# Performance work log

Measured on AMD Instinct MI355X. Metric: run time of the kernel, lower is better.

## Reference

```python
import jax, jax.numpy as jnp
import numpy as np
import math

EMBED_DIM = 1024
N_HEADS = 16
HEAD_DIM = EMBED_DIM // N_HEADS


def setup_inputs() -> dict:
    key = jax.random.key(0)
    k1, k2, k3, k4 = jax.random.split(key, 4)
    B, S, D = 2, 2048, EMBED_DIM
    inputs = jax.random.normal(k1, (B, S, D), dtype=jnp.float32)
    cross_embeddings = jax.random.normal(k2, (B, S, D), dtype=jnp.float32)
    # learned params
    ln_weight = jnp.ones((D,), dtype=jnp.float32)
    ln_bias = jnp.zeros((D,), dtype=jnp.float32)
    # nn.Linear weights are [out_features, in_features]
    kv_weight = jax.random.normal(k3, (2 * D, D), dtype=jnp.float32) * (1.0 / math.sqrt(D))
    q_weight = jax.random.normal(k4, (D, D), dtype=jnp.float32) * (1.0 / math.sqrt(D))
    return {
        "inputs": inputs,
        "cross_embeddings": cross_embeddings,
        "ln_weight": ln_weight,
        "ln_bias": ln_bias,
        "kv_weight": kv_weight,
        "q_weight": q_weight,
    }


def _layer_norm(x, w, b, eps=1e-5):
    mu = jnp.mean(x, axis=-1, keepdims=True)
    var = jnp.mean(jnp.square(x - mu), axis=-1, keepdims=True)
    return (x - mu) * jax.lax.rsqrt(var + eps) * w + b


def reference(inputs, cross_embeddings, ln_weight, ln_bias, kv_weight, q_weight):
    B, S, D = inputs.shape
    H, Dh = N_HEADS, HEAD_DIM
    resid = inputs
    x = _layer_norm(inputs, ln_weight, ln_bias)
    # kv projection on cross embeddings: y = x @ W^T
    kv = jnp.einsum('bsd,ed->bse', cross_embeddings, kv_weight)  # [B,S,2D]
    k, v = kv[..., :D], kv[..., D:]
    q = jnp.einsum('bsd,ed->bse', x, q_weight)  # [B,S,D]
    q = q.reshape(B, S, H, Dh).transpose(0, 2, 1, 3)  # [B,H,S,Dh]
    k = k.reshape(B, S, H, Dh).transpose(0, 2, 1, 3)
    v = v.reshape(B, S, H, Dh).transpose(0, 2, 1, 3)
    attn = jnp.einsum('bhqd,bhkd->bhqk', q, k) / math.sqrt(Dh)
    attn = jax.nn.softmax(attn, axis=-1)
    out = jnp.einsum('bhqk,bhkd->bhqd', attn, v)  # [B,H,S,Dh]
    out = out.transpose(0, 2, 1, 3).reshape(B, S, D)
    return out + resid
```

## Files before the change

### kernel.cpp

```cpp
#include <hip/hip_runtime.h>
#include <cstdint>
#include <cstddef>


typedef float  f32x4  __attribute__((ext_vector_type(4)));
typedef __bf16 bf16x8 __attribute__((ext_vector_type(8)));
typedef __bf16 bf16x4 __attribute__((ext_vector_type(4)));
typedef __bf16 bf16x2 __attribute__((ext_vector_type(2)));

#define MFMA16(a, b, c) __builtin_amdgcn_mfma_f32_16x16x32_bf16((a), (b), (c), 0, 0, 0)

__device__ __forceinline__ void gll16(const void* g, void* l) {
  __builtin_amdgcn_global_load_lds(
      (const __attribute__((address_space(1))) unsigned int*)g,
      (__attribute__((address_space(3))) unsigned int*)l, 16, 0, 0);
}

__device__ __forceinline__ bf16x2 split2(float x) {
  bf16x2 r;
  __bf16 hh = (__bf16)x;
  r[0] = hh;
  r[1] = (__bf16)(x - (float)hh);
  return r;
}

__global__ __launch_bounds__(256) void prep_kernel(
    const float* __restrict__ x, const float* __restrict__ w, const float* __restrict__ b,
    __bf16* __restrict__ xh, __bf16* __restrict__ xl,
    const float* __restrict__ c,  __bf16* __restrict__ ch, __bf16* __restrict__ cl,
    const float* __restrict__ kw, __bf16* __restrict__ kh, __bf16* __restrict__ kl,
    const float* __restrict__ qw, __bf16* __restrict__ qh, __bf16* __restrict__ ql)
{
  const int tid = threadIdx.x;
  if (blockIdx.x < 4096) {
    const int row = blockIdx.x;
    const float4 v = *reinterpret_cast<const float4*>(x + (size_t)row * 1024 + tid * 4);
    float s  = v.x + v.y + v.z + v.w;
    float s2 = v.x * v.x + v.y * v.y + v.z * v.z + v.w * v.w;
#pragma unroll
    for (int o = 1; o < 64; o <<= 1) { s += __shfl_xor(s, o, 64); s2 += __shfl_xor(s2, o, 64); }
    __shared__ float red[8];
    const int wv = tid >> 6, ln = tid & 63;
    if (ln == 0) { red[wv] = s; red[4 + wv] = s2; }
    __syncthreads();
    s  = red[0] + red[1] + red[2] + red[3];
    s2 = red[4] + red[5] + red[6] + red[7];
    const float mu = s * (1.f / 1024.f);
    const float rs = rsqrtf(s2 * (1.f / 1024.f) - mu * mu + 1e-5f);
    const float4 wv4 = *reinterpret_cast<const float4*>(w + tid * 4);
    const float4 bv4 = *reinterpret_cast<const float4*>(b + tid * 4);
    float o4[4] = {(v.x - mu) * rs * wv4.x + bv4.x, (v.y - mu) * rs * wv4.y + bv4.y,
                   (v.z - mu) * rs * wv4.z + bv4.z, (v.w - mu) * rs * wv4.w + bv4.w};
    bf16x4 h, l;
#pragma unroll
    for (int i = 0; i < 4; ++i) { bf16x2 hl = split2(o4[i]); h[i] = hl[0]; l[i] = hl[1]; }
    *reinterpret_cast<bf16x4*>(xh + (size_t)row * 1024 + tid * 4) = h;
    *reinterpret_cast<bf16x4*>(xl + (size_t)row * 1024 + tid * 4) = l;
  } else {
    const int i = ((blockIdx.x - 4096) * 256 + tid) * 4;
    const float* src; __bf16 *dh, *dl; int off;
    if (i < 4194304)      { src = c;  dh = ch; dl = cl; off = i; }
    else if (i < 6291456) { src = kw; dh = kh; dl = kl; off = i - 4194304; }
    else                  { src = qw; dh = qh; dl = ql; off = i - 6291456; }
    const float4 v = *reinterpret_cast<const float4*>(src + off);
    float o4[4] = {v.x, v.y, v.z, v.w};
    bf16x4 h, l;
#pragma unroll
    for (int j = 0; j < 4; ++j) { bf16x2 hl = split2(o4[j]); h[j] = hl[0]; l[j] = hl[1]; }
    *reinterpret_cast<bf16x4*>(dh + off) = h;
    *reinterpret_cast<bf16x4*>(dl + off) = l;
  }
}

__device__ __forceinline__ void gemm_tile(
    const __bf16* __restrict__ Ah, const __bf16* __restrict__ Al,
    const __bf16* __restrict__ Bh, const __bf16* __restrict__ Bl,
    __bf16* __restrict__ C, int N, int m0, int n0, char* ldsb)
{
  constexpr int K = 1024;
  const int tid  = threadIdx.x;
  const int wave = tid >> 6, lane = tid & 63;
  const int g = lane >> 4, qm = lane & 15;
  const int wr = wave >> 1, wc = wave & 1;

  f32x4 acc[4][4] = {};

  const int rr = tid >> 2;
  const int cc = tid & 3;
  const int wb = wave * 1024;

  for (int k0 = 0; k0 < K; k0 += 32) {
    const size_t a0 = (size_t)(m0 + rr) * K + k0 + cc * 8;
    const size_t a1 = (size_t)(m0 + 64 + rr) * K + k0 + cc * 8;
    const size_t b0 = (size_t)(n0 + rr) * K + k0 + cc * 8;
    const size_t b1 = (size_t)(n0 + 64 + rr) * K + k0 + cc * 8;
    gll16(Ah + a0, ldsb + 0     + wb);
    gll16(Ah + a1, ldsb + 4096  + wb);
    gll16(Al + a0, ldsb + 8192  + wb);
    gll16(Al + a1, ldsb + 12288 + wb);
    gll16(Bh + b0, ldsb + 16384 + wb);
    gll16(Bh + b1, ldsb + 20480 + wb);
    gll16(Bl + b0, ldsb + 24576 + wb);
    gll16(Bl + b1, ldsb + 28672 + wb);
    __syncthreads();

    bf16x8 bhf[4], blf[4];
#pragma unroll
    for (int nt = 0; nt < 4; ++nt) {
      const int brow = wc * 64 + nt * 16 + qm;
      const char* bp = ldsb + 16384 + brow * 64 + g * 16;
      bhf[nt] = *reinterpret_cast<const bf16x8*>(bp);
      blf[nt] = *reinterpret_cast<const bf16x8*>(bp + 8192);
    }
#pragma unroll
    for (int mt = 0; mt < 4; ++mt) {
      const int arow = wr * 64 + mt * 16 + qm;
      const char* ap = ldsb + arow * 64 + g * 16;
      const bf16x8 ahf = *reinterpret_cast<const bf16x8*>(ap);
      const bf16x8 alf = *reinterpret_cast<const bf16x8*>(ap + 8192);
#pragma unroll
      for (int nt = 0; nt < 4; ++nt) {
        acc[mt][nt] = MFMA16(ahf, bhf[nt], acc[mt][nt]);
        acc[mt][nt] = MFMA16(ahf, blf[nt], acc[mt][nt]);
        acc[mt][nt] = MFMA16(alf, bhf[nt], acc[mt][nt]);
      }
    }
    __syncthreads();
  }

#pragma unroll
  for (int mt = 0; mt < 4; ++mt)
#pragma unroll
    for (int nt = 0; nt < 4; ++nt) {
      const int col = n0 + wc * 64 + nt * 16 + qm;
#pragma unroll
      for (int r = 0; r < 4; ++r) {
        const int row = m0 + wr * 64 + mt * 16 + g * 4 + r;
        C[(size_t)row * N + col] = (__bf16)acc[mt][nt][r];
      }
    }
}

__global__ __launch_bounds__(256) void gemm2_kernel(
    const __bf16* __restrict__ cAh, const __bf16* __restrict__ cAl,
    const __bf16* __restrict__ kWh, const __bf16* __restrict__ kWl, __bf16* __restrict__ kvC,
    const __bf16* __restrict__ xAh, const __bf16* __restrict__ xAl,
    const __bf16* __restrict__ qWh, const __bf16* __restrict__ qWl, __bf16* __restrict__ qC)
{
  __shared__ __bf16 lds[4 * 128 * 32];
  int t = blockIdx.x;
  if (t < 512)
    gemm_tile(cAh, cAl, kWh, kWl, kvC, 2048, (t >> 4) * 128, (t & 15) * 128, (char*)lds);
  else {
    t -= 512;
    gemm_tile(xAh, xAl, qWh, qWl, qC, 1024, (t >> 3) * 128, (t & 7) * 128, (char*)lds);
  }
}

__global__ __launch_bounds__(256) void gemm1_kernel(
    const __bf16* __restrict__ Ah, const __bf16* __restrict__ Al,
    const __bf16* __restrict__ Bh, const __bf16* __restrict__ Bl,
    __bf16* __restrict__ C, int N)
{
  __shared__ __bf16 lds[4 * 128 * 32];
  gemm_tile(Ah, Al, Bh, Bl, C, N, blockIdx.y * 128, blockIdx.x * 128, (char*)lds);
}

__global__ __launch_bounds__(256) void attn_kernel(
    const __bf16* __restrict__ qb, const __bf16* __restrict__ kvb,
    const float* __restrict__ resid, float* __restrict__ out)
{
  const int bh = blockIdx.y, b = bh >> 4, h = bh & 15;
  const int q0 = blockIdx.x * 128;
  const int tid = threadIdx.x, wave = tid >> 6, lane = tid & 63;
  const int g = lane >> 4, qm = lane & 15;

  __shared__ __bf16 Kl[64 * 64];
  __shared__ __bf16 Vt[64 * 64];
  __shared__ __bf16 Pl[4][16 * 72];

  bf16x8 qf[2][2];
#pragma unroll
  for (int qs = 0; qs < 2; ++qs) {
    const size_t row = (size_t)(b * 2048 + q0 + qs * 64 + wave * 16 + qm);
    const __bf16* p = qb + row * 1024 + h * 64 + g * 8;
    qf[qs][0] = *reinterpret_cast<const bf16x8*>(p);
    qf[qs][1] = *reinterpret_cast<const bf16x8*>(p + 32);
  }

  float mrun[2][4], lrun[2][4];
#pragma unroll
  for (int qs = 0; qs < 2; ++qs)
#pragma unroll
    for (int r = 0; r < 4; ++r) { mrun[qs][r] = -1e30f; lrun[qs][r] = 0.f; }
  f32x4 acco[2][4] = {};
  const float scale = 0.125f;

  const int kr   = tid >> 3;
  const int kc   = tid & 7;
  const int kswz = kc ^ (kr & 7);

  for (int t = 0; t < 32; ++t) {
#pragma unroll
    for (int hh = 0; hh < 2; ++hh) {
      const int key = t * 64 + hh * 32 + kr;
      const __bf16* gp = kvb + (size_t)(b * 2048 + key) * 2048 + h * 64 + kswz * 8;
      gll16(gp, (char*)Kl + hh * 4096 + wave * 1024);
    }
#pragma unroll
    for (int it = 0; it < 2; ++it) {
      const int d0 = (wave + it * 4) * 8;
      const __bf16* gp = kvb + (size_t)(b * 2048 + t * 64 + lane) * 2048 + 1024 + h * 64 + d0;
      const bf16x8 v = *reinterpret_cast<const bf16x8*>(gp);
#pragma unroll
      for (int j = 0; j < 8; ++j) {
        const int d = d0 + j;
        const int ch = (lane >> 3) ^ (d & 7);
        Vt[d * 64 + ch * 8 + (lane & 7)] = v[j];
      }
    }
    __syncthreads();

#pragma unroll
    for (int qs = 0; qs < 2; ++qs) {
      f32x4 s[4] = {};
#pragma unroll
      for (int kt = 0; kt < 4; ++kt) {
        const int row = kt * 16 + qm;
#pragma unroll
        for (int kk = 0; kk < 2; ++kk) {
          const int ch = (kk * 4 + g) ^ (qm & 7);
          const bf16x8 kf = *reinterpret_cast<const bf16x8*>(&Kl[row * 64 + ch * 8]);
          s[kt] = MFMA16(qf[qs][kk], kf, s[kt]);
        }
      }

      float corr[4];
#pragma unroll
      for (int r = 0; r < 4; ++r) {
        float mx = fmaxf(fmaxf(s[0][r], s[1][r]), fmaxf(s[2][r], s[3][r]));
#pragma unroll
        for (int o = 1; o < 16; o <<= 1) mx = fmaxf(mx, __shfl_xor(mx, o, 64));
        mx *= scale;
        const float mn = fmaxf(mrun[qs][r], mx);
        corr[r] = __expf(mrun[qs][r] - mn);
        mrun[qs][r] = mn;
      }
#pragma unroll
      for (int r = 0; r < 4; ++r) {
        float ls = 0.f;
#pragma unroll
        for (int kt = 0; kt < 4; ++kt) {
          const float p = __expf(s[kt][r] * scale - mrun[qs][r]);
          ls += p;
          Pl[wave][(g * 4 + r) * 72 + kt * 16 + qm] = (__bf16)p;
        }
#pragma unroll
        for (int o = 1; o < 16; o <<= 1) ls += __shfl_xor(ls, o, 64);
        lrun[qs][r] = lrun[qs][r] * corr[r] + ls;
#pragma unroll
        for (int dt = 0; dt < 4; ++dt) acco[qs][dt][r] *= corr[r];
      }

#pragma unroll
      for (int ks = 0; ks < 2; ++ks) {
        const bf16x8 pf = *reinterpret_cast<const bf16x8*>(&Pl[wave][qm * 72 + ks * 32 + g * 8]);
#pragma unroll
        for (int dt = 0; dt < 4; ++dt) {
          const int drow = dt * 16 + qm;
          const int ch = (ks * 4 + g) ^ (qm & 7);
          const bf16x8 vf = *reinterpret_cast<const bf16x8*>(&Vt[drow * 64 + ch * 8]);
          acco[qs][dt] = MFMA16(pf, vf, acco[qs][dt]);
        }
      }
    }
    __syncthreads();
  }

#pragma unroll
  for (int qs = 0; qs < 2; ++qs)
#pragma unroll
    for (int dt = 0; dt < 4; ++dt) {
      const int col = h * 64 + dt * 16 + qm;
#pragma unroll
      for (int r = 0; r < 4; ++r) {
        const size_t tok = (size_t)(b * 2048 + q0 + qs * 64 + wave * 16 + g * 4 + r);
        out[tok * 1024 + col] = acco[qs][dt][r] / lrun[qs][r] + resid[tok * 1024 + col];
      }
    }
}

extern "C" void kernel_launch(void* const* d_in, const int* in_sizes, int n_in,
                              void* d_out, int out_size, void* d_ws, size_t ws_size,
                              hipStream_t stream)
{
  const float* inputs = (const float*)d_in[0];
  const float* cross  = (const float*)d_in[1];
  const float* lnw    = (const float*)d_in[2];
  const float* lnb    = (const float*)d_in[3];
  const float* kvw    = (const float*)d_in[4];
  const float* qw     = (const float*)d_in[5];
  float* out = (float*)d_out;

  char* ws = (char*)d_ws;
  const size_t MB = (size_t)1 << 20;
  __bf16* xh  = (__bf16*)(ws + 0 * MB);
  __bf16* xl  = (__bf16*)(ws + 8 * MB);
  __bf16* chh = (__bf16*)(ws + 16 * MB);
  __bf16* cll = (__bf16*)(ws + 24 * MB);
  __bf16* kwh = (__bf16*)(ws + 32 * MB);
  __bf16* kwl = (__bf16*)(ws + 36 * MB);
  __bf16* qwh = (__bf16*)(ws + 40 * MB);
  __bf16* qwl = (__bf16*)(ws + 42 * MB);
  __bf16* kvb = (__bf16*)(ws + 44 * MB);
  const bool merged = ws_size >= 68 * MB;
  __bf16* qbb = merged ? (__bf16*)(ws + 60 * MB) : (__bf16*)(ws + 16 * MB);

  prep_kernel<<<11264, 256, 0, stream>>>(inputs, lnw, lnb, xh, xl,
                                         cross, chh, cll, kvw, kwh, kwl, qw, qwh, qwl);
  if (merged) {
    gemm2_kernel<<<768, 256, 0, stream>>>(chh, cll, kwh, kwl, kvb,
                                          xh, xl, qwh, qwl, qbb);
  } else {
    gemm1_kernel<<<dim3(16, 32), 256, 0, stream>>>(chh, cll, kwh, kwl, kvb, 2048);
    gemm1_kernel<<<dim3(8, 32), 256, 0, stream>>>(xh, xl, qwh, qwl, qbb, 1024);
  }
  attn_kernel<<<dim3(16, 32), 256, 0, stream>>>(qbb, kvb, inputs, out);
}
```

Measured before the change: 305.4 us.

## Double-buffer K/V tiles in attention and use 8 waves per block

The attention kernel now launches 512 threads, so each of 8 waves owns 16 query rows instead of 4 waves handling 32 rows each. K and V tiles are double-buffered in LDS: the next tile's K is fetched asynchronously and its V is loaded into registers while the current tile is processed, and only one barrier per iteration remains. Softmax now uses exp2f with a log2e-folded scale. The aim is to hide global-load latency and raise occupancy, at the cost of more LDS per block and Q-fragment-to-K reuse halved per wave.

```diff
diff --git a/kernel.cpp b/kernel.cpp
--- a/kernel.cpp
+++ b/kernel.cpp
@@ -166,7 +166,7 @@
   gemm_tile(Ah, Al, Bh, Bl, C, N, blockIdx.y * 128, blockIdx.x * 128, (char*)lds);
 }
 
-__global__ __launch_bounds__(256) void attn_kernel(
+__global__ __launch_bounds__(512) void attn_kernel(
     const __bf16* __restrict__ qb, const __bf16* __restrict__ kvb,
     const float* __restrict__ resid, float* __restrict__ out)
 {
@@ -175,119 +175,124 @@
   const int tid = threadIdx.x, wave = tid >> 6, lane = tid & 63;
   const int g = lane >> 4, qm = lane & 15;
 
-  __shared__ __bf16 Kl[64 * 64];
-  __shared__ __bf16 Vt[64 * 64];
-  __shared__ __bf16 Pl[4][16 * 72];
-
-  bf16x8 qf[2][2];
-#pragma unroll
-  for (int qs = 0; qs < 2; ++qs) {
-    const size_t row = (size_t)(b * 2048 + q0 + qs * 64 + wave * 16 + qm);
+  __shared__ __bf16 Kl[2][64 * 64];
+  __shared__ __bf16 Vt[2][64 * 64];
+  __shared__ __bf16 Pl[8][16 * 72];
+
+  bf16x8 qf[2];
+  {
+    const size_t row = (size_t)(b * 2048 + q0 + wave * 16 + qm);
     const __bf16* p = qb + row * 1024 + h * 64 + g * 8;
-    qf[qs][0] = *reinterpret_cast<const bf16x8*>(p);
-    qf[qs][1] = *reinterpret_cast<const bf16x8*>(p + 32);
-  }
-
-  float mrun[2][4], lrun[2][4];
-#pragma unroll
-  for (int qs = 0; qs < 2; ++qs)
-#pragma unroll
-    for (int r = 0; r < 4; ++r) { mrun[qs][r] = -1e30f; lrun[qs][r] = 0.f; }
-  f32x4 acco[2][4] = {};
-  const float scale = 0.125f;
-
-  const int kr   = tid >> 3;
-  const int kc   = tid & 7;
-  const int kswz = kc ^ (kr & 7);
+    qf[0] = *reinterpret_cast<const bf16x8*>(p);
+    qf[1] = *reinterpret_cast<const bf16x8*>(p + 32);
+  }
+
+  float mrun[4], lrun[4];
+#pragma unroll
+  for (int r = 0; r < 4; ++r) { mrun[r] = -1e30f; lrun[r] = 0.f; }
+  f32x4 acco[4] = {};
+  const float scale2 = 0.125f * 1.44269504f;
+
+  const int krow  = wave * 8 + (lane >> 3);
+  const int kchnk = (lane & 7) ^ (krow & 7);
+  const int vd0 = wave * 8;
+
+  const size_t kv_base = (size_t)(b * 2048) * 2048 + h * 64;
+
+  gll16(kvb + kv_base + (size_t)krow * 2048 + kchnk * 8, (char*)Kl[0] + wave * 1024);
+  bf16x8 vreg = *reinterpret_cast<const bf16x8*>(
+      kvb + kv_base + (size_t)lane * 2048 + 1024 + vd0);
+  {
+#pragma unroll
+    for (int j = 0; j < 8; ++j) {
+      const int d = vd0 + j;
+      const int ch = (lane >> 3) ^ (d & 7);
+      Vt[0][d * 64 + ch * 8 + (lane & 7)] = vreg[j];
+    }
+  }
+  __syncthreads();
 
   for (int t = 0; t < 32; ++t) {
-#pragma unroll
-    for (int hh = 0; hh < 2; ++hh) {
-      const int key = t * 64 + hh * 32 + kr;
-      const __bf16* gp = kvb + (size_t)(b * 2048 + key) * 2048 + h * 64 + kswz * 8;
-      gll16(gp, (char*)Kl + hh * 4096 + wave * 1024);
-    }
-#pragma unroll
-    for (int it = 0; it < 2; ++it) {
-      const int d0 = (wave + it * 4) * 8;
-      const __bf16* gp = kvb + (size_t)(b * 2048 + t * 64 + lane) * 2048 + 1024 + h * 64 + d0;
-      const bf16x8 v = *reinterpret_cast<const bf16x8*>(gp);
+    const int cur = t & 1, nxt = cur ^ 1;
+    if (t < 31) {
+      const size_t key0 = (size_t)(t + 1) * 64;
+      gll16(kvb + kv_base + (key0 + krow) * 2048 + kchnk * 8,
+            (char*)Kl[nxt] + wave * 1024);
+      vreg = *reinterpret_cast<const bf16x8*>(
+          kvb + kv_base + (key0 + lane) * 2048 + 1024 + vd0);
+    }
+
+    f32x4 s[4] = {};
+#pragma unroll
+    for (int kt = 0; kt < 4; ++kt) {
+      const int row = kt * 16 + qm;
+#pragma unroll
+      for (int kk = 0; kk < 2; ++kk) {
+        const int ch = (kk * 4 + g) ^ (qm & 7);
+        const bf16x8 kf = *reinterpret_cast<const bf16x8*>(&Kl[cur][row * 64 + ch * 8]);
+        s[kt] = MFMA16(qf[kk], kf, s[kt]);
+      }
+    }
+
+    float corr[4];
+#pragma unroll
+    for (int r = 0; r < 4; ++r) {
+      float mx = fmaxf(fmaxf(s[0][r], s[1][r]), fmaxf(s[2][r], s[3][r]));
+#pragma unroll
+      for (int o = 1; o < 16; o <<= 1) mx = fmaxf(mx, __shfl_xor(mx, o, 64));
+      mx *= scale2;
+      const float mn = fmaxf(mrun[r], mx);
+      corr[r] = exp2f(mrun[r] - mn);
+      mrun[r] = mn;
+    }
+#pragma unroll
+    for (int r = 0; r < 4; ++r) {
+      float ls = 0.f;
+#pragma unroll
+      for (int kt = 0; kt < 4; ++kt) {
+        const float p = exp2f(s[kt][r] * scale2 - mrun[r]);
+        ls += p;
+        Pl[wave][(g * 4 + r) * 72 + kt * 16 + qm] = (__bf16)p;
+      }
+#pragma unroll
+      for (int o = 1; o < 16; o <<= 1) ls += __shfl_xor(ls, o, 64);
+      lrun[r] = lrun[r] * corr[r] + ls;
+#pragma unroll
+      for (int dt = 0; dt < 4; ++dt) acco[dt][r] *= corr[r];
+    }
+
+#pragma unroll
+    for (int ks = 0; ks < 2; ++ks) {
+      const bf16x8 pf = *reinterpret_cast<const bf16x8*>(&Pl[wave][qm * 72 + ks * 32 + g * 8]);
+#pragma unroll
+      for (int dt = 0; dt < 4; ++dt) {
+        const int drow = dt * 16 + qm;
+        const int ch = (ks * 4 + g) ^ (qm & 7);
+        const bf16x8 vf = *reinterpret_cast<const bf16x8*>(&Vt[cur][drow * 64 + ch * 8]);
+        acco[dt] = MFMA16(pf, vf, acco[dt]);
+      }
+    }
+
+    if (t < 31) {
 #pragma unroll
       for (int j = 0; j < 8; ++j) {
-        const int d = d0 + j;
+        const int d = vd0 + j;
         const int ch = (lane >> 3) ^ (d & 7);
-        Vt[d * 64 + ch * 8 + (lane & 7)] = v[j];
+        Vt[nxt][d * 64 + ch * 8 + (lane & 7)] = vreg[j];
       }
     }
     __syncthreads();
-
-#pragma unroll
-    for (int qs = 0; qs < 2; ++qs) {
-      f32x4 s[4] = {};
-#pragma unroll
-      for (int kt = 0; kt < 4; ++kt) {
-        const int row = kt * 16 + qm;
-#pragma unroll
-        for (int kk = 0; kk < 2; ++kk) {
-          const int ch = (kk * 4 + g) ^ (qm & 7);
-          const bf16x8 kf = *reinterpret_cast<const bf16x8*>(&Kl[row * 64 + ch * 8]);
-          s[kt] = MFMA16(qf[qs][kk], kf, s[kt]);
-        }
-      }
-
-      float corr[4];
-#pragma unroll
-      for (int r = 0; r < 4; ++r) {
-        float mx = fmaxf(fmaxf(s[0][r], s[1][r]), fmaxf(s[2][r], s[3][r]));
-#pragma unroll
-        for (int o = 1; o < 16; o <<= 1) mx = fmaxf(mx, __shfl_xor(mx, o, 64));
-        mx *= scale;
-        const float mn = fmaxf(mrun[qs][r], mx);
-        corr[r] = __expf(mrun[qs][r] - mn);
-        mrun[qs][r] = mn;
-      }
-#pragma unroll
-      for (int r = 0; r < 4; ++r) {
-        float ls = 0.f;
-#pragma unroll
-        for (int kt = 0; kt < 4; ++kt) {
-          const float p = __expf(s[kt][r] * scale - mrun[qs][r]);
-          ls += p;
-          Pl[wave][(g * 4 + r) * 72 + kt * 16 + qm] = (__bf16)p;
-        }
-#pragma unroll
-        for (int o = 1; o < 16; o <<= 1) ls += __shfl_xor(ls, o, 64);
-        lrun[qs][r] = lrun[qs][r] * corr[r] + ls;
-#pragma unroll
-        for (int dt = 0; dt < 4; ++dt) acco[qs][dt][r] *= corr[r];
-      }
-
-#pragma unroll
-      for (int ks = 0; ks < 2; ++ks) {
-        const bf16x8 pf = *reinterpret_cast<const bf16x8*>(&Pl[wave][qm * 72 + ks * 32 + g * 8]);
-#pragma unroll
-        for (int dt = 0; dt < 4; ++dt) {
-          const int drow = dt * 16 + qm;
-          const int ch = (ks * 4 + g) ^ (qm & 7);
-          const bf16x8 vf = *reinterpret_cast<const bf16x8*>(&Vt[drow * 64 + ch * 8]);
-          acco[qs][dt] = MFMA16(pf, vf, acco[qs][dt]);
-        }
-      }
-    }
-    __syncthreads();
-  }
-
-#pragma unroll
-  for (int qs = 0; qs < 2; ++qs)
-#pragma unroll
-    for (int dt = 0; dt < 4; ++dt) {
-      const int col = h * 64 + dt * 16 + qm;
-#pragma unroll
-      for (int r = 0; r < 4; ++r) {
-        const size_t tok = (size_t)(b * 2048 + q0 + qs * 64 + wave * 16 + g * 4 + r);
-        out[tok * 1024 + col] = acco[qs][dt][r] / lrun[qs][r] + resid[tok * 1024 + col];
-      }
-    }
+  }
+
+#pragma unroll
+  for (int dt = 0; dt < 4; ++dt) {
+    const int col = h * 64 + dt * 16 + qm;
+#pragma unroll
+    for (int r = 0; r < 4; ++r) {
+      const size_t tok = (size_t)(b * 2048 + q0 + wave * 16 + g * 4 + r);
+      out[tok * 1024 + col] = acco[dt][r] / lrun[r] + resid[tok * 1024 + col];
+    }
+  }
 }
 
 extern "C" void kernel_launch(void* const* d_in, const int* in_sizes, int n_in,
@@ -325,5 +330,5 @@
     gemm1_kernel<<<dim3(16, 32), 256, 0, stream>>>(chh, cll, kwh, kwl, kvb, 2048);
     gemm1_kernel<<<dim3(8, 32), 256, 0, stream>>>(xh, xl, qwh, qwl, qbb, 1024);
   }
-  attn_kernel<<<dim3(16, 32), 256, 0, stream>>>(qbb, kvb, inputs, out);
-}
+  attn_kernel<<<dim3(16, 32), 512, 0, stream>>>(qbb, kvb, inputs, out);
+}
```

Measured after the change: 294.5 us. 3.6% less time.
